# Performance work log

Measured on AMD Instinct MI355X. Metric: run time of the kernel, lower is better.

The kernel has to match this reference:

```python
import jax, jax.numpy as jnp
import numpy as np

N_EMBD = 384
N_HEADS = 6
HEAD_SIZE = N_EMBD // N_HEADS  # 64
LN_EPS = 1e-5


def _layernorm(x, g, b):
    mu = jnp.mean(x, axis=-1, keepdims=True)
    var = jnp.var(x, axis=-1, keepdims=True)
    return (x - mu) * jax.lax.rsqrt(var + LN_EPS) * g + b


def setup_inputs() -> dict:
    key = jax.random.key(0)
    ks = jax.random.split(key, 12)
    B, T, C, H, D = 128, 256, N_EMBD, N_HEADS, HEAD_SIZE
    s_in = 1.0 / np.sqrt(C)
    s_ff = 1.0 / np.sqrt(4 * C)
    return {
        "x": jax.random.normal(ks[0], (B, T, C), dtype=jnp.float32),
        "ln1_g": jnp.ones((C,), jnp.float32),
        "ln1_b": jnp.zeros((C,), jnp.float32),
        "Wq": jax.random.uniform(ks[1], (H, C, D), jnp.float32, -s_in, s_in),
        "Wk": jax.random.uniform(ks[2], (H, C, D), jnp.float32, -s_in, s_in),
        "Wv": jax.random.uniform(ks[3], (H, C, D), jnp.float32, -s_in, s_in),
        "Wo": jax.random.uniform(ks[4], (C, C), jnp.float32, -s_in, s_in),
        "bo": jnp.zeros((C,), jnp.float32),
        "ln2_g": jnp.ones((C,), jnp.float32),
        "ln2_b": jnp.zeros((C,), jnp.float32),
        "W1": jax.random.uniform(ks[5], (C, 4 * C), jnp.float32, -s_in, s_in),
        "b1": jnp.zeros((4 * C,), jnp.float32),
        "W2": jax.random.uniform(ks[6], (4 * C, C), jnp.float32, -s_ff, s_ff),
        "b2": jnp.zeros((C,), jnp.float32),
    }


def reference(x, ln1_g, ln1_b, Wq, Wk, Wv, Wo, bo, ln2_g, ln2_b, W1, b1, W2, b2):
    # Dropout layers are identity (eval mode).
    B, T, C = x.shape
    h = _layernorm(x, ln1_g, ln1_b)
    # Per-head projections: [B,T,C] x [H,C,D] -> [B,H,T,D]
    q = jnp.einsum('btc,hcd->bhtd', h, Wq)
    k = jnp.einsum('btc,hcd->bhtd', h, Wk)
    v = jnp.einsum('btc,hcd->bhtd', h, Wv)
    scale = HEAD_SIZE ** (-0.5)
    scores = jnp.einsum('bhtd,bhsd->bhts', q, k) * scale  # [B,H,T,T]
    causal = jnp.tril(jnp.ones((T, T), dtype=bool))
    scores = jnp.where(causal, scores, jnp.float32(-jnp.inf))
    wei = jax.nn.softmax(scores, axis=-1)
    attn = jnp.einsum('bhts,bhsd->bhtd', wei, v)  # [B,H,T,D]
    attn = attn.transpose(0, 2, 1, 3).reshape(B, T, C)  # concat heads
    x = x + attn @ Wo + bo
    h2 = _layernorm(x, ln2_g, ln2_b)
    ff = jax.nn.relu(h2 @ W1 + b1) @ W2 + b2
    return x + ff
```

## Files before the change

kernel.cpp:

```cpp
#include <hip/hip_runtime.h>

typedef unsigned int u32;
typedef unsigned short u16;
typedef __bf16 bf16_t;
typedef float f32x4 __attribute__((ext_vector_type(4)));
typedef bf16_t bfrag __attribute__((ext_vector_type(8)));
typedef u16 u16x8 __attribute__((ext_vector_type(8)));

__device__ inline u16 f2bf(float f) {
    union { float f; u32 u; } v; v.f = f;
    u32 r = v.u + 0x7fffu + ((v.u >> 16) & 1u);
    return (u16)(r >> 16);
}
__device__ inline float bf2f(u16 h) {
    union { u32 u; float f; } v; v.u = ((u32)h) << 16; return v.f;
}

__device__ inline f32x4 mfma16(bfrag a, bfrag b, f32x4 c) {
    return __builtin_amdgcn_mfma_f32_16x16x32_bf16(a, b, c, 0, 0, 0);
}

__device__ inline void gload_lds16(const void* g, void* l) {
    __builtin_amdgcn_global_load_lds((const __attribute__((address_space(1))) u32*)g,
                                     (__attribute__((address_space(3))) u32*)l, 16, 0, 0);
}

__device__ inline float redmax16(float v) {
    #pragma unroll
    for (int m = 1; m < 16; m <<= 1) v = fmaxf(v, __shfl_xor(v, m));
    return v;
}
__device__ inline float redsum16(float v) {
    #pragma unroll
    for (int m = 1; m < 16; m <<= 1) v += __shfl_xor(v, m);
    return v;
}

#define NTOK 32768
#define QKV_ELEMS 12582912

__global__ __launch_bounds__(256) void prep_weights(
    const float* __restrict__ Wq, const float* __restrict__ Wk,
    const float* __restrict__ Wv, const float* __restrict__ Wo,
    const float* __restrict__ W1, const float* __restrict__ W2,
    u16* __restrict__ wqkvT, u16* __restrict__ woT,
    u16* __restrict__ w1T, u16* __restrict__ w2T)
{
    __shared__ float tile[64][65];
    const int b = blockIdx.x;
    const float* src; u16* dst;
    int sr0, sc0, srs, dr0, dc0, drs;
    if (b < 36) {
        int i = b / 6, j = b - i * 6;
        src = Wo;  srs = 384;  sr0 = i * 64; sc0 = j * 64;
        dst = woT; drs = 384;  dr0 = j * 64; dc0 = i * 64;
    } else if (b < 180) {
        int t = b - 36; int i = t / 24, j = t - i * 24;
        src = W1;  srs = 1536; sr0 = i * 64; sc0 = j * 64;
        dst = w1T; drs = 384;  dr0 = j * 64; dc0 = i * 64;
    } else if (b < 324) {
        int t = b - 180; int i = t / 6, j = t - i * 6;
        src = W2;  srs = 384;  sr0 = i * 64; sc0 = j * 64;
        dst = w2T; drs = 1536; dr0 = j * 64; dc0 = i * 64;
    } else {
        int t = b - 324;
        int m2 = t / 36; t -= m2 * 36;
        int h = t / 6, tt = t - h * 6;
        src = (m2 == 0) ? Wq : ((m2 == 1) ? Wk : Wv);
        srs = 64;  sr0 = h * 384 + tt * 64; sc0 = 0;
        dst = wqkvT; drs = 384; dr0 = m2 * 384 + h * 64; dc0 = tt * 64;
    }
    const int lane = threadIdx.x & 63, grp = threadIdx.x >> 6;
    #pragma unroll
    for (int i = 0; i < 16; i++) {
        int r = grp * 16 + i;
        tile[r][lane] = src[(size_t)(sr0 + r) * srs + sc0 + lane];
    }
    __syncthreads();
    #pragma unroll
    for (int i = 0; i < 16; i++) {
        int r = grp * 16 + i;
        dst[(size_t)(dr0 + r) * drs + dc0 + lane] = f2bf(tile[lane][r]);
    }
}

__global__ __launch_bounds__(256) void ln_f32(
    const float* __restrict__ x, const float* __restrict__ g,
    const float* __restrict__ b, u16* __restrict__ out)
{
    const int row = blockIdx.x * 4 + (threadIdx.x >> 6);
    const int lane = threadIdx.x & 63;
    const float2* xr = (const float2*)(x + (size_t)row * 384);
    float2 v[3];
    float s = 0.f, s2 = 0.f;
    #pragma unroll
    for (int i = 0; i < 3; i++) {
        v[i] = xr[lane + i * 64];
        s += v[i].x + v[i].y; s2 += v[i].x * v[i].x + v[i].y * v[i].y;
    }
    #pragma unroll
    for (int m = 1; m < 64; m <<= 1) { s += __shfl_xor(s, m); s2 += __shfl_xor(s2, m); }
    float mean = s * (1.f / 384.f);
    float rstd = rsqrtf(s2 * (1.f / 384.f) - mean * mean + 1e-5f);
    u32* op = (u32*)(out + (size_t)row * 384);
    #pragma unroll
    for (int i = 0; i < 3; i++) {
        int c = (lane + i * 64) * 2;
        u32 lo = f2bf((v[i].x - mean) * rstd * g[c] + b[c]);
        u32 hi = f2bf((v[i].y - mean) * rstd * g[c + 1] + b[c + 1]);
        op[lane + i * 64] = lo | (hi << 16);
    }
}

__global__ __launch_bounds__(256) void ln_bf16(
    const u16* __restrict__ x, const float* __restrict__ g,
    const float* __restrict__ b, u16* __restrict__ out)
{
    const int row = blockIdx.x * 4 + (threadIdx.x >> 6);
    const int lane = threadIdx.x & 63;
    const u32* xr = (const u32*)(x + (size_t)row * 384);
    float vx[3], vy[3];
    float s = 0.f, s2 = 0.f;
    #pragma unroll
    for (int i = 0; i < 3; i++) {
        u32 w = xr[lane + i * 64];
        vx[i] = bf2f((u16)(w & 0xffffu));
        vy[i] = bf2f((u16)(w >> 16));
        s += vx[i] + vy[i]; s2 += vx[i] * vx[i] + vy[i] * vy[i];
    }
    #pragma unroll
    for (int m = 1; m < 64; m <<= 1) { s += __shfl_xor(s, m); s2 += __shfl_xor(s2, m); }
    float mean = s * (1.f / 384.f);
    float rstd = rsqrtf(s2 * (1.f / 384.f) - mean * mean + 1e-5f);
    u32* op = (u32*)(out + (size_t)row * 384);
    #pragma unroll
    for (int i = 0; i < 3; i++) {
        int c = (lane + i * 64) * 2;
        u32 lo = f2bf((vx[i] - mean) * rstd * g[c] + b[c]);
        u32 hi = f2bf((vy[i] - mean) * rstd * g[c + 1] + b[c + 1]);
        op[lane + i * 64] = lo | (hi << 16);
    }
}

template<int EPI, int NBN>
__global__ __launch_bounds__(512, 1) void gemm_pb(
    const u16* __restrict__ A, const u16* __restrict__ Bt,
    const float* __restrict__ bias, const void* __restrict__ resid,
    void* __restrict__ outp, int G_CNT)
{
    const int K = 384, NKC = 6, N = NBN * 128;
    __shared__ __align__(16) u16 smem[73728];
    u16* Bs = smem;
    u16* Ar = smem + 49152;
    const int tid = threadIdx.x, wave = tid >> 6, lane = tid & 63;
    const int lr = lane >> 3, lc = lane & 7;
    const int nwg = gridDim.x, bid = blockIdx.x;
    const int qx = nwg >> 3, rx = nwg & 7, xc = bid & 7, ii = bid >> 3;
    const int wg = (xc < rx ? xc * (qx + 1) : rx * (qx + 1) + (xc - rx) * qx) + ii;
    const int g = wg / NBN, bn = wg - g * NBN;
    const int rowB0 = bn << 7;
    const int wm = (wave >> 1) << 5, wn = (wave & 1) << 6;

    #pragma unroll
    for (int s = 0; s < NKC; s++)
        #pragma unroll
        for (int p = 0; p < 2; p++) {
            const int idx = p * 8 + wave;
            const int r = idx * 8 + lr;
            gload_lds16(Bt + (size_t)(rowB0 + r) * K + s * 64 + ((lc ^ (r & 7)) << 3),
                        &Bs[s * 8192 + idx * 512]);
        }
    asm volatile("s_waitcnt vmcnt(0)" ::: "memory");
    __syncthreads();

    const int ntiles = (256 - g + G_CNT - 1) / G_CNT;
    const int U = ntiles * NKC;
    f32x4 acc[2][4] = {};

#define STAGE_A(u)                                                                   \
    {                                                                                \
        const int t_ = (u) / NKC, s_ = (u) - t_ * NKC, sl_ = (u) % 3;                \
        const int rA0_ = (g + t_ * G_CNT) << 7;                                      \
        _Pragma("unroll")                                                            \
        for (int p = 0; p < 2; p++) {                                                \
            const int idx = p * 8 + wave;                                            \
            const int r = idx * 8 + lr;                                              \
            gload_lds16(A + (size_t)(rA0_ + r) * K + s_ * 64 + ((lc ^ (r & 7)) << 3),\
                        &Ar[sl_ * 8192 + idx * 512]);                                \
        }                                                                            \
    }

    STAGE_A(0);
    if (U > 1) STAGE_A(1);

    for (int u = 0; u < U; ++u) {
        if (u + 2 < U) {
            STAGE_A(u + 2);
            asm volatile("s_waitcnt vmcnt(4)" ::: "memory");
        } else if (u + 1 < U) {
            asm volatile("s_waitcnt vmcnt(2)" ::: "memory");
        } else {
            asm volatile("s_waitcnt vmcnt(0)" ::: "memory");
        }
        __builtin_amdgcn_s_barrier();
        const int s = u % NKC;
        const char* Ab = (const char*)&Ar[(u % 3) * 8192];
        const char* Bb = (const char*)&Bs[s * 8192];
        #pragma unroll
        for (int kk = 0; kk < 2; kk++) {
            bfrag af[2], bfr[4];
            #pragma unroll
            for (int mt = 0; mt < 2; mt++) {
                const int row = wm + mt * 16 + (lane & 15);
                af[mt] = *(const bfrag*)(Ab + row * 128 +
                          (((kk * 4 + (lane >> 4)) ^ (row & 7)) << 4));
            }
            #pragma unroll
            for (int nt = 0; nt < 4; nt++) {
                const int row = wn + nt * 16 + (lane & 15);
                bfr[nt] = *(const bfrag*)(Bb + row * 128 +
                          (((kk * 4 + (lane >> 4)) ^ (row & 7)) << 4));
            }
            #pragma unroll
            for (int mt = 0; mt < 2; mt++)
                #pragma unroll
                for (int nt = 0; nt < 4; nt++)
                    acc[mt][nt] = mfma16(af[mt], bfr[nt], acc[mt][nt]);
        }
        if (s == NKC - 1) {
            const int rowA0 = (g + (u / NKC) * G_CNT) << 7;
            #pragma unroll
            for (int mt = 0; mt < 2; mt++) {
                #pragma unroll
                for (int nt = 0; nt < 4; nt++) {
                    #pragma unroll
                    for (int r2 = 0; r2 < 4; r2++) {
                        const int gr = rowA0 + wm + mt * 16 + ((lane >> 4) << 2) + r2;
                        const int gc = rowB0 + wn + nt * 16 + (lane & 15);
                        float v = acc[mt][nt][r2];
                        if constexpr (EPI == 0) {
                            int m2 = gc / 384;
                            int rem = gc - m2 * 384;
                            int hh = rem >> 6, d = rem & 63;
                            if (m2 == 0) v *= 0.125f;
                            int bb = gr >> 8, t2 = gr & 255;
                            ((u16*)outp)[(size_t)m2 * QKV_ELEMS +
                                         ((size_t)((bb * 6 + hh) * 256 + t2) << 6) + d] = f2bf(v);
                        } else if constexpr (EPI == 1) {
                            ((u16*)outp)[(size_t)gr * N + gc] =
                                f2bf(((const float*)resid)[(size_t)gr * N + gc] + bias[gc] + v);
                        } else {
                            float t2 = v + bias[gc];
                            ((u16*)outp)[(size_t)gr * N + gc] = f2bf(t2 > 0.f ? t2 : 0.f);
                        }
                    }
                    acc[mt][nt] = (f32x4){0.f, 0.f, 0.f, 0.f};
                }
            }
        }
        __builtin_amdgcn_s_barrier();
    }
#undef STAGE_A
}

template<int EPI, int NT>
__global__ __launch_bounds__(256, 4) void gemm_m97(
    const u16* __restrict__ A, const u16* __restrict__ Bt,
    const float* __restrict__ bias, const void* __restrict__ resid,
    void* __restrict__ outp, int M, int N)
{
    const int K = NT * 64;
    __shared__ __align__(16) u16 As[128 * 64];
    __shared__ __align__(16) u16 Bs[128 * 64];
    const int tid = threadIdx.x, wave = tid >> 6, lane = tid & 63;
    const int nbn = N >> 7;
    const int nwg = gridDim.x;
    const int bid = blockIdx.x;
    const int wg = (bid & 7) * (nwg >> 3) + (bid >> 3);
    const int bm = wg / nbn, bn = wg - bm * nbn;
    const int rowA0 = bm << 7, rowB0 = bn << 7;
    const int wm = (wave >> 1) << 6, wn = (wave & 1) << 6;
    const int lr = lane >> 3, lc = lane & 7;
    f32x4 acc[4][4] = {};

    for (int t = 0; t < NT; ++t) {
        const int ko = t << 6;
        #pragma unroll
        for (int p = 0; p < 4; p++) {
            const int idx = p * 4 + wave;
            const int r = idx * 8 + lr;
            const int csrc = ((lc ^ (r & 7)) << 3);
            gload_lds16(A + (size_t)(rowA0 + r) * K + ko + csrc, &As[idx * 512]);
            gload_lds16(Bt + (size_t)(rowB0 + r) * K + ko + csrc, &Bs[idx * 512]);
        }
        __syncthreads();
        #pragma unroll
        for (int kk = 0; kk < 2; kk++) {
            bfrag af[4], bfr[4];
            #pragma unroll
            for (int mt = 0; mt < 4; mt++) {
                const int row = wm + mt * 16 + (lane & 15);
                af[mt] = *(const bfrag*)((const char*)As + row * 128 +
                          (((kk * 4 + (lane >> 4)) ^ (row & 7)) << 4));
            }
            #pragma unroll
            for (int nt = 0; nt < 4; nt++) {
                const int row = wn + nt * 16 + (lane & 15);
                bfr[nt] = *(const bfrag*)((const char*)Bs + row * 128 +
                          (((kk * 4 + (lane >> 4)) ^ (row & 7)) << 4));
            }
            #pragma unroll
            for (int mt = 0; mt < 4; mt++)
                #pragma unroll
                for (int nt = 0; nt < 4; nt++)
                    acc[mt][nt] = mfma16(af[mt], bfr[nt], acc[mt][nt]);
        }
        __syncthreads();
    }

    #pragma unroll
    for (int mt = 0; mt < 4; mt++) {
        #pragma unroll
        for (int nt = 0; nt < 4; nt++) {
            #pragma unroll
            for (int r2 = 0; r2 < 4; r2++) {
                const int gr = rowA0 + wm + mt * 16 + ((lane >> 4) << 2) + r2;
                const int gc = rowB0 + wn + nt * 16 + (lane & 15);
                float v = acc[mt][nt][r2];
                ((float*)outp)[(size_t)gr * N + gc] =
                    bf2f(((const u16*)resid)[(size_t)gr * N + gc]) + bias[gc] + v;
            }
        }
    }
}

__global__ __launch_bounds__(512) void attn_kernel(
    const u16* __restrict__ q, const u16* __restrict__ k, const u16* __restrict__ v,
    u16* __restrict__ outp)
{
    __shared__ __align__(16) u16 Ks[256 * 64];
    __shared__ __align__(16) u16 Vt[64 * 256];
    __shared__ __align__(16) u16 Ps[8 * 512];
    const int bh = blockIdx.x;
    const int tid = threadIdx.x, wave = tid >> 6, lane = tid & 63;
    const u16* qb = q + (size_t)bh * 16384;
    const u16* kb = k + (size_t)bh * 16384;
    const u16* vb = v + (size_t)bh * 16384;

    #pragma unroll
    for (int p = 0; p < 4; p++) {
        const int idx = p * 8 + wave;
        const int r = idx * 8 + (lane >> 3);
        const int csrc = (((lane & 7) ^ (r & 7)) << 3);
        gload_lds16(kb + (size_t)r * 64 + csrc, &Ks[idx * 512]);
    }
    #pragma unroll
    for (int p = 0; p < 4; p++) {
        const int e = (p * 512 + tid) * 8;
        const int key = e >> 6, d0 = e & 63;
        u16x8 raw = *(const u16x8*)(vb + (size_t)key * 64 + d0);
        #pragma unroll
        for (int j = 0; j < 8; j++) {
            const int d = d0 + j;
            Vt[d * 256 + (((key >> 3) ^ (d & 7)) << 3) + (key & 7)] = raw[j];
        }
    }
    __syncthreads();

    const int bI = bh / 6, hh = bh - bI * 6;

    #pragma unroll
    for (int t = 0; t < 2; t++) {
        const int qtile = (t == 0) ? wave : (15 - wave);
        const int qrowbase = qtile * 16;
        bfrag qf[2];
        {
            const int r = qrowbase + (lane & 15);
            qf[0] = *(const bfrag*)(qb + (size_t)r * 64 + ((lane >> 4) << 3));
            qf[1] = *(const bfrag*)(qb + (size_t)r * 64 + 32 + ((lane >> 4) << 3));
        }
        f32x4 S[16];
        #pragma unroll
        for (int kt = 0; kt < 16; kt++) {
            if (kt <= qtile) {
                f32x4 s = {0.f, 0.f, 0.f, 0.f};
                const int key = kt * 16 + (lane & 15);
                const char* kbase = (const char*)Ks + key * 128;
                s = mfma16(qf[0], *(const bfrag*)(kbase + ((((lane >> 4)) ^ (key & 7)) << 4)), s);
                s = mfma16(qf[1], *(const bfrag*)(kbase + (((4 + (lane >> 4)) ^ (key & 7)) << 4)), s);
                if (kt == qtile) {
                    const int qit = (lane >> 4) << 2;
                    #pragma unroll
                    for (int r2 = 0; r2 < 4; r2++)
                        if ((lane & 15) > qit + r2) s[r2] = -1e30f;
                }
                S[kt] = s;
            }
        }
        float mx[4] = {-1e30f, -1e30f, -1e30f, -1e30f};
        #pragma unroll
        for (int kt = 0; kt < 16; kt++) if (kt <= qtile)
            #pragma unroll
            for (int r2 = 0; r2 < 4; r2++) mx[r2] = fmaxf(mx[r2], S[kt][r2]);
        #pragma unroll
        for (int r2 = 0; r2 < 4; r2++) mx[r2] = redmax16(mx[r2]);
        float sm[4] = {0.f, 0.f, 0.f, 0.f};
        #pragma unroll
        for (int kt = 0; kt < 16; kt++) if (kt <= qtile)
            #pragma unroll
            for (int r2 = 0; r2 < 4; r2++) {
                float p = __expf(S[kt][r2] - mx[r2]);
                S[kt][r2] = p; sm[r2] += p;
            }
        #pragma unroll
        for (int r2 = 0; r2 < 4; r2++) sm[r2] = redsum16(sm[r2]);

        f32x4 O[4] = {};
        u16* Pw = &Ps[wave * 512];
        const int nch = (qtile + 2) >> 1;
        #pragma unroll
        for (int ch = 0; ch < 8; ch++) {
            if (ch < nch) {
                #pragma unroll
                for (int ktl = 0; ktl < 2; ktl++) {
                    const int kt = ch * 2 + ktl;
                    const int keyl = ktl * 16 + (lane & 15);
                    const int cidx = keyl >> 3;
                    #pragma unroll
                    for (int r2 = 0; r2 < 4; r2++) {
                        const int qq = ((lane >> 4) << 2) + r2;
                        float pv = (kt <= qtile) ? S[kt][r2] : 0.f;
                        Pw[qq * 32 + ((cidx ^ (qq & 3)) << 3) + (keyl & 7)] = f2bf(pv);
                    }
                }
                const int qq = lane & 15;
                bfrag pa = *(const bfrag*)(Pw + qq * 32 + (((lane >> 4) ^ (qq & 3)) << 3));
                #pragma unroll
                for (int dt = 0; dt < 4; dt++) {
                    const int d = dt * 16 + (lane & 15);
                    const int cc = ch * 4 + (lane >> 4);
                    bfrag vf = *(const bfrag*)((const char*)Vt + d * 512 + ((cc ^ (d & 7)) << 4));
                    O[dt] = mfma16(pa, vf, O[dt]);
                }
            }
        }
        #pragma unroll
        for (int dt = 0; dt < 4; dt++) {
            #pragma unroll
            for (int r2 = 0; r2 < 4; r2++) {
                const int qg = qrowbase + ((lane >> 4) << 2) + r2;
                const float val = O[dt][r2] / sm[r2];
                outp[(size_t)(bI * 256 + qg) * 384 + hh * 64 + dt * 16 + (lane & 15)] = f2bf(val);
            }
        }
    }
}

extern "C" void kernel_launch(void* const* d_in, const int* in_sizes, int n_in,
                              void* d_out, int out_size, void* d_ws, size_t ws_size,
                              hipStream_t stream)
{
    const float* x    = (const float*)d_in[0];
    const float* ln1g = (const float*)d_in[1];
    const float* ln1b = (const float*)d_in[2];
    const float* Wq   = (const float*)d_in[3];
    const float* Wk   = (const float*)d_in[4];
    const float* Wv   = (const float*)d_in[5];
    const float* Wo   = (const float*)d_in[6];
    const float* bo   = (const float*)d_in[7];
    const float* ln2g = (const float*)d_in[8];
    const float* ln2b = (const float*)d_in[9];
    const float* W1   = (const float*)d_in[10];
    const float* b1   = (const float*)d_in[11];
    const float* W2   = (const float*)d_in[12];
    const float* b2   = (const float*)d_in[13];

    if (ws_size < 230031360u) return;

    char* ws = (char*)d_ws;
    u16*   wqkvT = (u16*)(ws + 0);
    u16*   woT   = (u16*)(ws + 884736);
    u16*   w1T   = (u16*)(ws + 1179648);
    u16*   w2T   = (u16*)(ws + 2359296);
    u16*   hbuf  = (u16*)(ws + 3538944);
    u16*   qbuf  = (u16*)(ws + 28704768);
    u16*   kbuf  = (u16*)(ws + 53870592);
    u16*   vbuf  = (u16*)(ws + 79036416);
    u16*   x2h   = (u16*)(ws + 104202240);
    u16*   mid   = (u16*)(ws + 129368064);
    float* out   = (float*)d_out;

    prep_weights<<<432, 256, 0, stream>>>(Wq, Wk, Wv, Wo, W1, W2, wqkvT, woT, w1T, w2T);
    ln_f32<<<8192, 256, 0, stream>>>(x, ln1g, ln1b, hbuf);
    gemm_pb<0, 9><<<252, 512, 0, stream>>>(hbuf, wqkvT, nullptr, nullptr, qbuf, 28);
    attn_kernel<<<768, 512, 0, stream>>>(qbuf, kbuf, vbuf, hbuf);
    gemm_pb<1, 3><<<255, 512, 0, stream>>>(hbuf, woT, bo, x, x2h, 85);
    ln_bf16<<<8192, 256, 0, stream>>>(x2h, ln2g, ln2b, qbuf);
    gemm_pb<2, 12><<<252, 512, 0, stream>>>(qbuf, w1T, b1, nullptr, mid, 21);
    gemm_m97<3, 24><<<768, 256, 0, stream>>>(mid, w2T, b2, x2h, out, NTOK, 384);
}
```

Before: 260.6 us.

## Move residual and bias add from Wo GEMM epilogue into LN2 kernel

The Wo projection GEMM now writes only the raw bf16 product to a scratch buffer. The residual read of x plus bo and the bf16 x2 store move into a new fused residual+layernorm kernel that also emits the LN2 output. This takes the strided fp32 residual loads out of the GEMM epilogue. The FFN1 GEMM also preloads its per-lane bias values into registers, and the A-stage wait count is relaxed at tile boundaries (vmcnt 36) so epilogue stores need not drain before compute. In exchange the product is rounded to bf16 before the residual add, which adds some extra rounding error.

```diff
diff --git a/kernel.cpp b/kernel.cpp
--- a/kernel.cpp
+++ b/kernel.cpp
@@ -112,33 +112,39 @@
     }
 }
 
-__global__ __launch_bounds__(256) void ln_bf16(
-    const u16* __restrict__ x, const float* __restrict__ g,
-    const float* __restrict__ b, u16* __restrict__ out)
+__global__ __launch_bounds__(256) void ln_resid(
+    const float* __restrict__ x, const u16* __restrict__ wout,
+    const float* __restrict__ bo, const float* __restrict__ g,
+    const float* __restrict__ b, u16* __restrict__ x2h, u16* __restrict__ h2)
 {
     const int row = blockIdx.x * 4 + (threadIdx.x >> 6);
     const int lane = threadIdx.x & 63;
-    const u32* xr = (const u32*)(x + (size_t)row * 384);
-    float vx[3], vy[3];
+    const float2* xr = (const float2*)(x + (size_t)row * 384);
+    const u32* wr = (const u32*)(wout + (size_t)row * 384);
+    float tx[3], ty[3];
     float s = 0.f, s2 = 0.f;
     #pragma unroll
     for (int i = 0; i < 3; i++) {
-        u32 w = xr[lane + i * 64];
-        vx[i] = bf2f((u16)(w & 0xffffu));
-        vy[i] = bf2f((u16)(w >> 16));
-        s += vx[i] + vy[i]; s2 += vx[i] * vx[i] + vy[i] * vy[i];
+        float2 xv = xr[lane + i * 64];
+        u32 w = wr[lane + i * 64];
+        int c = (lane + i * 64) * 2;
+        tx[i] = xv.x + bf2f((u16)(w & 0xffffu)) + bo[c];
+        ty[i] = xv.y + bf2f((u16)(w >> 16)) + bo[c + 1];
+        s += tx[i] + ty[i]; s2 += tx[i] * tx[i] + ty[i] * ty[i];
     }
     #pragma unroll
     for (int m = 1; m < 64; m <<= 1) { s += __shfl_xor(s, m); s2 += __shfl_xor(s2, m); }
     float mean = s * (1.f / 384.f);
     float rstd = rsqrtf(s2 * (1.f / 384.f) - mean * mean + 1e-5f);
-    u32* op = (u32*)(out + (size_t)row * 384);
+    u32* xo = (u32*)(x2h + (size_t)row * 384);
+    u32* ho = (u32*)(h2 + (size_t)row * 384);
     #pragma unroll
     for (int i = 0; i < 3; i++) {
         int c = (lane + i * 64) * 2;
-        u32 lo = f2bf((vx[i] - mean) * rstd * g[c] + b[c]);
-        u32 hi = f2bf((vy[i] - mean) * rstd * g[c + 1] + b[c + 1]);
-        op[lane + i * 64] = lo | (hi << 16);
+        xo[lane + i * 64] = (u32)f2bf(tx[i]) | ((u32)f2bf(ty[i]) << 16);
+        u32 lo = f2bf((tx[i] - mean) * rstd * g[c] + b[c]);
+        u32 hi = f2bf((ty[i] - mean) * rstd * g[c + 1] + b[c + 1]);
+        ho[lane + i * 64] = lo | (hi << 16);
     }
 }
 
@@ -161,6 +167,13 @@
     const int rowB0 = bn << 7;
     const int wm = (wave >> 1) << 5, wn = (wave & 1) << 6;
 
+    float bias4[4] = {0.f, 0.f, 0.f, 0.f};
+    if constexpr (EPI == 2) {
+        #pragma unroll
+        for (int nt = 0; nt < 4; nt++)
+            bias4[nt] = bias[rowB0 + wn + nt * 16 + (lane & 15)];
+    }
+
     #pragma unroll
     for (int s = 0; s < NKC; s++)
         #pragma unroll
@@ -194,16 +207,20 @@
     if (U > 1) STAGE_A(1);
 
     for (int u = 0; u < U; ++u) {
+        const int s = u % NKC;
         if (u + 2 < U) {
             STAGE_A(u + 2);
-            asm volatile("s_waitcnt vmcnt(4)" ::: "memory");
+            if (u >= NKC && s <= 1) {
+                asm volatile("s_waitcnt vmcnt(36)" ::: "memory");
+            } else {
+                asm volatile("s_waitcnt vmcnt(4)" ::: "memory");
+            }
         } else if (u + 1 < U) {
             asm volatile("s_waitcnt vmcnt(2)" ::: "memory");
         } else {
             asm volatile("s_waitcnt vmcnt(0)" ::: "memory");
         }
         __builtin_amdgcn_s_barrier();
-        const int s = u % NKC;
         const char* Ab = (const char*)&Ar[(u % 3) * 8192];
         const char* Bb = (const char*)&Bs[s * 8192];
         #pragma unroll
@@ -247,10 +264,9 @@
                             ((u16*)outp)[(size_t)m2 * QKV_ELEMS +
                                          ((size_t)((bb * 6 + hh) * 256 + t2) << 6) + d] = f2bf(v);
                         } else if constexpr (EPI == 1) {
-                            ((u16*)outp)[(size_t)gr * N + gc] =
-                                f2bf(((const float*)resid)[(size_t)gr * N + gc] + bias[gc] + v);
+                            ((u16*)outp)[(size_t)gr * N + gc] = f2bf(v);
                         } else {
-                            float t2 = v + bias[gc];
+                            float t2 = v + bias4[nt];
                             ((u16*)outp)[(size_t)gr * N + gc] = f2bf(t2 > 0.f ? t2 : 0.f);
                         }
                     }
@@ -494,8 +510,8 @@
     ln_f32<<<8192, 256, 0, stream>>>(x, ln1g, ln1b, hbuf);
     gemm_pb<0, 9><<<252, 512, 0, stream>>>(hbuf, wqkvT, nullptr, nullptr, qbuf, 28);
     attn_kernel<<<768, 512, 0, stream>>>(qbuf, kbuf, vbuf, hbuf);
-    gemm_pb<1, 3><<<255, 512, 0, stream>>>(hbuf, woT, bo, x, x2h, 85);
-    ln_bf16<<<8192, 256, 0, stream>>>(x2h, ln2g, ln2b, qbuf);
+    gemm_pb<1, 3><<<255, 512, 0, stream>>>(hbuf, woT, nullptr, nullptr, kbuf, 85);
+    ln_resid<<<8192, 256, 0, stream>>>(x, kbuf, bo, ln2g, ln2b, x2h, qbuf);
     gemm_pb<2, 12><<<252, 512, 0, stream>>>(qbuf, w1T, b1, nullptr, mid, 21);
     gemm_m97<3, 24><<<768, 256, 0, stream>>>(mid, w2T, b2, x2h, out, NTOK, 384);
 }
```

Result: slower. 267.5 us (+2.7%).
